# Kernel optimization log

Measured on AMD Instinct MI355X. Metric: run time of the kernel, lower is better.

The kernel has to match this reference:

```python
import jax, jax.numpy as jnp
import numpy as np

B, N, C, E, K, L = 8, 20000, 256, 320000, 3, 2
EPS = 1e-5

def setup_inputs() -> dict:
    key = jax.random.key(0)
    ks = jax.random.split(key, 8)
    features = jax.random.normal(ks[0], (B * N, C), dtype=jnp.float32)
    edge_index = jax.random.randint(ks[1], (2, E), 0, N, dtype=jnp.int64)
    # ChebConv params per layer: K linear weights [C,C] (no per-lin bias) + one bias [C]
    W = jax.random.normal(ks[2], (L, K, C, C), dtype=jnp.float32) * 0.05
    b = jax.random.normal(ks[3], (L, C), dtype=jnp.float32) * 0.05
    # node-mode LayerNorm affine params per layer
    ln_w = jnp.ones((L, C), dtype=jnp.float32)
    ln_b = jnp.zeros((L, C), dtype=jnp.float32)
    return {"features": features, "W": W, "b": b, "ln_w": ln_w, "ln_b": ln_b,
            "edge_index": edge_index, "batch_size": B}


def reference(features, W, b, ln_w, ln_b, edge_index, batch_size):
    n = features.shape[0] // batch_size
    c = features.shape[-1]
    src, dst = edge_index[0], edge_index[1]
    # sym-normalized Laplacian, lambda_max=2: L_hat = 2L/lmax - I = -D^-1/2 A D^-1/2
    deg = jax.ops.segment_sum(jnp.ones_like(src, dtype=features.dtype), src, num_segments=n)
    dis = jnp.where(deg > 0, jax.lax.rsqrt(jnp.where(deg > 0, deg, 1.0)), 0.0)
    norm = -dis[src] * dis[dst]  # [E]
    n_layers, k_order = W.shape[0], W.shape[1]

    def prop(x):  # L_hat @ x via gather-scale-scatter
        return jax.ops.segment_sum(norm[:, None] * x[src], dst, num_segments=n)

    def cheb(x, Wl, bl):
        Tx0 = x
        out = Tx0 @ Wl[0]
        Tx1 = prop(Tx0)
        out = out + Tx1 @ Wl[1]
        for k in range(2, k_order):
            Tx2 = 2.0 * prop(Tx1) - Tx0
            out = out + Tx2 @ Wl[k]
            Tx0, Tx1 = Tx1, Tx2
        return out + bl

    def single(feats):  # [n, c] -> [n, c]
        x = feats
        for i in range(n_layers):
            # NOTE: module passes original features to every layer's conv (faithful)
            x = cheb(feats, W[i], b[i])
            mu = jnp.mean(x, axis=-1, keepdims=True)
            var = jnp.var(x, axis=-1, keepdims=True)
            x = (x - mu) * jax.lax.rsqrt(var + EPS) * ln_w[i] + ln_b[i]
            # dropout p=0.0 -> identity
        return x

    fb = features.reshape(batch_size, n, c)
    return jax.vmap(single)(fb)
```

## Files before the change

### kernel.cpp

```cpp
#include <hip/hip_runtime.h>
#include <stdint.h>

#define BB 8
#define NN 20000
#define CC 256
#define EE 320000
#define KK 3
#define MROWS (BB * NN)
#define ROWU (BB * CC)

__device__ __forceinline__ float bf2f(ushort u) {
    union { uint32_t ui; float f; } v; v.ui = ((uint32_t)u) << 16; return v.f;
}
__device__ __forceinline__ ushort f2bf(float f) {
    union { uint32_t ui; float f; } v; v.f = f;
    uint32_t r = (v.ui + 0x7FFFu + ((v.ui >> 16) & 1u)) >> 16;
    return (ushort)r;
}

typedef __bf16 bf16x8 __attribute__((ext_vector_type(8)));
typedef float  f32x4  __attribute__((ext_vector_type(4)));

__device__ __forceinline__ void gload16(const void* gptr, void* lptr) {
    __builtin_amdgcn_global_load_lds(
        (const __attribute__((address_space(1))) void*)gptr,
        (__attribute__((address_space(3))) void*)lptr, 16, 0, 0);
}

__global__ void detect_k(const int* __restrict__ raw, int* __restrict__ flag) {
    int i = blockIdx.x * 256 + threadIdx.x;
    int v = 0;
    int idx = 2 * i + 1;
    if (i < EE) v = raw[idx];
    unsigned long long m = __ballot(v != 0);
    if ((threadIdx.x & 63) == 0 && m) atomicOr(flag, 1);
}

__global__ void convcount_k(const int* __restrict__ raw, const int* __restrict__ flag,
                            int mode,
                            int* __restrict__ src, int* __restrict__ dst,
                            int* __restrict__ deg_out, int* __restrict__ cnt_in) {
    int e = blockIdx.x * 256 + threadIdx.x;
    if (e >= EE) return;
    int m = mode ? mode : (*flag ? 1 : 2);
    int s, d;
    if (m == 2) { s = raw[2 * e]; d = raw[2 * EE + 2 * e]; }
    else        { s = raw[e];     d = raw[EE + e]; }
    src[e] = s; dst[e] = d;
    atomicAdd(&deg_out[s], 1);
    atomicAdd(&cnt_in[d], 1);
}

__global__ void __launch_bounds__(1024) scan_k(const int* __restrict__ cnt_in,
                                               const int* __restrict__ deg_out,
                                               int* __restrict__ row_ptr,
                                               float* __restrict__ dis) {
    __shared__ int wpart[16];
    const int t = threadIdx.x;
    const int lane = t & 63, wid = t >> 6;
    const int base = t * 20;
    int local[20];
    int sum = 0;
#pragma unroll
    for (int i = 0; i < 20; i++) {
        int idx = base + i;
        int v = (idx < NN) ? cnt_in[idx] : 0;
        local[i] = sum;
        sum += v;
    }
    int sc = sum;
#pragma unroll
    for (int off = 1; off < 64; off <<= 1) {
        int u = __shfl_up(sc, off, 64);
        if (lane >= off) sc += u;
    }
    if (lane == 63) wpart[wid] = sc;
    __syncthreads();
    if (wid == 0 && lane < 16) {
        int v = wpart[lane];
#pragma unroll
        for (int off = 1; off < 16; off <<= 1) {
            int u = __shfl_up(v, off, 64);
            if (lane >= off) v += u;
        }
        wpart[lane] = v;
    }
    __syncthreads();
    int wbase = (wid > 0) ? wpart[wid - 1] : 0;
    int tbase = wbase + sc - sum;
#pragma unroll
    for (int i = 0; i < 20; i++) {
        int idx = base + i;
        if (idx < NN) row_ptr[idx] = tbase + local[i];
    }
    if (t == 1023) row_ptr[NN] = tbase + sum;
    for (int i = t; i < NN; i += 1024) {
        int d = deg_out[i];
        dis[i] = (d > 0) ? rsqrtf((float)d) : 0.0f;
    }
}

__global__ void fill_k(const int* __restrict__ src, const int* __restrict__ dst,
                       const int* __restrict__ row_ptr, int* __restrict__ fillc,
                       const float* __restrict__ dis,
                       int2* __restrict__ cw) {
    int e = blockIdx.x * 256 + threadIdx.x;
    if (e >= EE) return;
    int s = src[e], d = dst[e];
    int pos = row_ptr[d] + atomicAdd(&fillc[d], 1);
    cw[pos] = make_int2(s, __float_as_int(-dis[s] * dis[d]));
}

__global__ void cvtwprep_k(const float* __restrict__ x, ushort* __restrict__ y,
                           const float* __restrict__ W, ushort* __restrict__ wt) {
    int bid = blockIdx.x;
    if (bid < MROWS * CC / 1024) {
        size_t idx = ((size_t)bid * 256 + threadIdx.x) * 4;
        int row = (int)(idx >> 8);
        int c = (int)(idx & 255);
        int b = row / NN, n = row - b * NN;
        float4 v = *(const float4*)(x + idx);
        ushort4 o = make_ushort4(f2bf(v.x), f2bf(v.y), f2bf(v.z), f2bf(v.w));
        *(ushort4*)(y + ((size_t)(n * BB + b) * CC + c)) = o;
    } else {
        int idx = (bid - MROWS * CC / 1024) * 256 + threadIdx.x;
        if (idx >= 256 * 768) return;
        int n = idx / 768, k = idx % 768;
        int sel = k >> 8, kk = k & 255;
        const float* W1 = W + KK * CC * CC;
        float v;
        if (sel == 0)      v = W1[kk * CC + n] - W1[2 * CC * CC + kk * CC + n];
        else if (sel == 1) v = W1[CC * CC + kk * CC + n];
        else               v = 2.0f * W1[2 * CC * CC + kk * CC + n];
        wt[idx] = f2bf(v);
    }
}

__global__ void __launch_bounds__(256) prop_k(const ushort* __restrict__ x,
                                              ushort* __restrict__ y,
                                              const int* __restrict__ row_ptr,
                                              const int2* __restrict__ cw) {
    const int n = blockIdx.x;
    const int t = threadIdx.x;
    const int beg = row_ptr[n], end = row_ptr[n + 1];
    const ushort* xb = x + t * 8;
    float a0 = 0, a1 = 0, a2 = 0, a3 = 0, a4 = 0, a5 = 0, a6 = 0, a7 = 0;
    int j = beg;
    for (; j + 4 <= end; j += 4) {
        int2 e0 = cw[j], e1 = cw[j + 1], e2 = cw[j + 2], e3 = cw[j + 3];
        int s0 = e0.x, s1 = e1.x, s2 = e2.x, s3 = e3.x;
        float w0 = __int_as_float(e0.y), w1 = __int_as_float(e1.y);
        float w2 = __int_as_float(e2.y), w3 = __int_as_float(e3.y);
        uint4 v0 = *(const uint4*)(xb + (size_t)s0 * ROWU);
        uint4 v1 = *(const uint4*)(xb + (size_t)s1 * ROWU);
        uint4 v2 = *(const uint4*)(xb + (size_t)s2 * ROWU);
        uint4 v3 = *(const uint4*)(xb + (size_t)s3 * ROWU);
        a0 += w0 * bf2f((ushort)v0.x) + w1 * bf2f((ushort)v1.x) + w2 * bf2f((ushort)v2.x) + w3 * bf2f((ushort)v3.x);
        a1 += w0 * bf2f((ushort)(v0.x >> 16)) + w1 * bf2f((ushort)(v1.x >> 16)) + w2 * bf2f((ushort)(v2.x >> 16)) + w3 * bf2f((ushort)(v3.x >> 16));
        a2 += w0 * bf2f((ushort)v0.y) + w1 * bf2f((ushort)v1.y) + w2 * bf2f((ushort)v2.y) + w3 * bf2f((ushort)v3.y);
        a3 += w0 * bf2f((ushort)(v0.y >> 16)) + w1 * bf2f((ushort)(v1.y >> 16)) + w2 * bf2f((ushort)(v2.y >> 16)) + w3 * bf2f((ushort)(v3.y >> 16));
        a4 += w0 * bf2f((ushort)v0.z) + w1 * bf2f((ushort)v1.z) + w2 * bf2f((ushort)v2.z) + w3 * bf2f((ushort)v3.z);
        a5 += w0 * bf2f((ushort)(v0.z >> 16)) + w1 * bf2f((ushort)(v1.z >> 16)) + w2 * bf2f((ushort)(v2.z >> 16)) + w3 * bf2f((ushort)(v3.z >> 16));
        a6 += w0 * bf2f((ushort)v0.w) + w1 * bf2f((ushort)v1.w) + w2 * bf2f((ushort)v2.w) + w3 * bf2f((ushort)v3.w);
        a7 += w0 * bf2f((ushort)(v0.w >> 16)) + w1 * bf2f((ushort)(v1.w >> 16)) + w2 * bf2f((ushort)(v2.w >> 16)) + w3 * bf2f((ushort)(v3.w >> 16));
    }
    for (; j < end; j++) {
        int2 e0 = cw[j];
        int s = e0.x;
        float wt = __int_as_float(e0.y);
        uint4 v = *(const uint4*)(xb + (size_t)s * ROWU);
        a0 += wt * bf2f((ushort)v.x);
        a1 += wt * bf2f((ushort)(v.x >> 16));
        a2 += wt * bf2f((ushort)v.y);
        a3 += wt * bf2f((ushort)(v.y >> 16));
        a4 += wt * bf2f((ushort)v.z);
        a5 += wt * bf2f((ushort)(v.z >> 16));
        a6 += wt * bf2f((ushort)v.w);
        a7 += wt * bf2f((ushort)(v.w >> 16));
    }
    uint4 o;
    o.x = (uint32_t)f2bf(a0) | ((uint32_t)f2bf(a1) << 16);
    o.y = (uint32_t)f2bf(a2) | ((uint32_t)f2bf(a3) << 16);
    o.z = (uint32_t)f2bf(a4) | ((uint32_t)f2bf(a5) << 16);
    o.w = (uint32_t)f2bf(a6) | ((uint32_t)f2bf(a7) << 16);
    *(uint4*)(y + (size_t)n * ROWU + t * 8) = o;
}

#define STAGE(buf, kt_) do {                                                   \
    const ushort* ab_ = ((kt_) < 8) ? a0 : (((kt_) < 16) ? a1 : a2);           \
    const int kl_ = ((kt_) & 7) * 32;                                          \
    const int kg_ = (kt_) * 32;                                                \
    gload16(ab_ + (size_t)(row0 + (tid >> 2)) * CC + kl_ + (tid & 3) * 8,      \
            &As[buf][wid * 512]);                                              \
    gload16(wt + (size_t)(tid >> 2) * 768 + kg_ + (tid & 3) * 8,               \
            &Bs[buf][wid * 512]);                                              \
    gload16(wt + (size_t)((512 + tid) >> 2) * 768 + kg_ + (tid & 3) * 8,       \
            &Bs[buf][4096 + wid * 512]);                                       \
} while (0)

__global__ void __launch_bounds__(512, 4) gemmln_k(const ushort* __restrict__ a0,
                                                   const ushort* __restrict__ a1,
                                                   const ushort* __restrict__ a2,
                                                   const ushort* __restrict__ wt,
                                                   const float* __restrict__ bias,
                                                   const float* __restrict__ lnw,
                                                   const float* __restrict__ lnb,
                                                   float* __restrict__ out) {
    __shared__ ushort As[2][128 * 32];
    __shared__ ushort Bs[2][256 * 32];
    __shared__ float reds[128][4];
    __shared__ float redq[128][4];
    const int tid = threadIdx.x;
    const int wid = tid >> 6, lane = tid & 63;
    const int wrow = wid >> 2, wcol = wid & 3;
    const int quad = lane >> 4, l16 = lane & 15;
    const int row0 = blockIdx.x * 128;

    f32x4 acc[4][4] = {};

    STAGE(0, 0);
    __syncthreads();
    int cur = 0;
    for (int kt = 0; kt < 24; kt++) {
        if (kt < 23) STAGE(cur ^ 1, kt + 1);

        bf16x8 af[4], bfr[4];
#pragma unroll
        for (int mt = 0; mt < 4; mt++)
            af[mt] = *(const bf16x8*)&As[cur][(wrow * 64 + mt * 16 + l16) * 32 + quad * 8];
#pragma unroll
        for (int nt = 0; nt < 4; nt++)
            bfr[nt] = *(const bf16x8*)&Bs[cur][(wcol * 64 + nt * 16 + l16) * 32 + quad * 8];
#pragma unroll
        for (int mt = 0; mt < 4; mt++)
#pragma unroll
            for (int nt = 0; nt < 4; nt++)
                acc[mt][nt] = __builtin_amdgcn_mfma_f32_16x16x32_bf16(
                    af[mt], bfr[nt], acc[mt][nt], 0, 0, 0);

        __syncthreads();
        cur ^= 1;
    }

    float bv[4], lwv[4], lbv[4];
#pragma unroll
    for (int nt = 0; nt < 4; nt++) {
        int c = wcol * 64 + nt * 16 + l16;
        bv[nt] = bias[c]; lwv[nt] = lnw[c]; lbv[nt] = lnb[c];
    }
#pragma unroll
    for (int mt = 0; mt < 4; mt++) {
#pragma unroll
        for (int r = 0; r < 4; r++) {
            float s = 0.0f, q = 0.0f;
#pragma unroll
            for (int nt = 0; nt < 4; nt++) {
                float v = acc[mt][nt][r] + bv[nt];
                s += v; q += v * v;
            }
#pragma unroll
            for (int off = 1; off < 16; off <<= 1) {
                s += __shfl_xor(s, off, 64);
                q += __shfl_xor(q, off, 64);
            }
            if (l16 == 0) {
                int ml = wrow * 64 + mt * 16 + quad * 4 + r;
                reds[ml][wcol] = s;
                redq[ml][wcol] = q;
            }
        }
    }
    __syncthreads();
#pragma unroll
    for (int mt = 0; mt < 4; mt++) {
#pragma unroll
        for (int r = 0; r < 4; r++) {
            int ml = wrow * 64 + mt * 16 + quad * 4 + r;
            float s = reds[ml][0] + reds[ml][1] + reds[ml][2] + reds[ml][3];
            float q = redq[ml][0] + redq[ml][1] + redq[ml][2] + redq[ml][3];
            float mean = s * (1.0f / CC);
            float var = q * (1.0f / CC) - mean * mean;
            float rs = rsqrtf(var + 1e-5f);
            int m = row0 + ml;
            int n = m >> 3, b = m & 7;
            size_t orow = (size_t)b * NN + n;
#pragma unroll
            for (int nt = 0; nt < 4; nt++) {
                int c = wcol * 64 + nt * 16 + l16;
                float v = (acc[mt][nt][r] + bv[nt] - mean) * rs * lwv[nt] + lbv[nt];
                out[orow * CC + c] = v;
            }
        }
    }
}

extern "C" void kernel_launch(void* const* d_in, const int* in_sizes, int n_in,
                              void* d_out, int out_size, void* d_ws, size_t ws_size,
                              hipStream_t stream) {
    const float* feats = (const float*)d_in[0];
    const float* W     = (const float*)d_in[1];
    const float* bvec  = (const float*)d_in[2];
    const float* lnw   = (const float*)d_in[3];
    const float* lnb   = (const float*)d_in[4];
    const int*   eidx  = (const int*)d_in[5];
    float* outp = (float*)d_out;

    int* flag    = (int*)d_ws;
    int* deg_out = flag + 64;
    int* cnt_in  = deg_out + NN;
    int* fillc   = cnt_in + NN;
    int* row_ptr = fillc + NN;
    int* srcw    = row_ptr + (NN + 64);
    int* dstw    = srcw + EE;
    int2* cw     = (int2*)(dstw + EE);
    float* disw  = (float*)(cw + EE);
    uintptr_t bf_base = ((uintptr_t)(disw + NN + 64) + 255) & ~(uintptr_t)255;
    ushort* featsb = (ushort*)bf_base;
    ushort* tx1b   = featsb + (size_t)MROWS * CC;
    ushort* p2b    = tx1b + (size_t)MROWS * CC;
    ushort* wcat   = p2b + (size_t)MROWS * CC;

    hipMemsetAsync(flag, 0, (size_t)(64 + 3 * NN) * sizeof(int), stream);

    int mode = 0;
    long long esz = in_sizes ? (long long)in_sizes[5] : 0;
    if (esz == (long long)2 * EE * 8) mode = 2;
    else if (esz == (long long)2 * EE * 4) mode = 1;

    int eb = (EE + 255) / 256;
    if (mode == 0) detect_k<<<eb, 256, 0, stream>>>(eidx, flag);
    convcount_k<<<eb, 256, 0, stream>>>(eidx, flag, mode, srcw, dstw, deg_out, cnt_in);
    scan_k<<<1, 1024, 0, stream>>>(cnt_in, deg_out, row_ptr, disw);
    fill_k<<<eb, 256, 0, stream>>>(srcw, dstw, row_ptr, fillc, disw, cw);

    cvtwprep_k<<<MROWS * CC / 1024 + 768, 256, 0, stream>>>(feats, featsb, W, wcat);

    prop_k<<<NN, 256, 0, stream>>>(featsb, tx1b, row_ptr, cw);
    prop_k<<<NN, 256, 0, stream>>>(tx1b, p2b, row_ptr, cw);

    gemmln_k<<<MROWS / 128, 512, 0, stream>>>(featsb, tx1b, p2b, wcat,
                                              bvec + CC, lnw + CC, lnb + CC, outp);
}
```

Before: 911.2 us.

## Switch bf16 activations to batch-major layout and fuse preprocessing kernels

Node activations now stay in the original batch-major [B][N][C] layout instead of being interleaved node-major [N][B][C]. The propagation kernel is restructured to one wavefront per (node, batch) pair on a 2D grid, with each lane gathering 8 bytes per neighbor instead of 16. The edge conversion/degree counting, feature bf16 conversion and weight prep are merged into a single launch, and the GEMM epilogue writes rows directly. The old node-major layout let each neighbor gather pull all batches as one contiguous 4 KB row. The new layout trades that for 512-byte gathers per neighbor and rereads the edge list once per batch, in exchange for a simpler transpose-free conversion and one fewer launch.

```diff
diff --git a/kernel.cpp b/kernel.cpp
--- a/kernel.cpp
+++ b/kernel.cpp
@@ -7,7 +7,6 @@
 #define EE 320000
 #define KK 3
 #define MROWS (BB * NN)
-#define ROWU (BB * CC)
 
 __device__ __forceinline__ float bf2f(ushort u) {
     union { uint32_t ui; float f; } v; v.ui = ((uint32_t)u) << 16; return v.f;
@@ -36,19 +35,39 @@
     if ((threadIdx.x & 63) == 0 && m) atomicOr(flag, 1);
 }
 
-__global__ void convcount_k(const int* __restrict__ raw, const int* __restrict__ flag,
-                            int mode,
-                            int* __restrict__ src, int* __restrict__ dst,
-                            int* __restrict__ deg_out, int* __restrict__ cnt_in) {
-    int e = blockIdx.x * 256 + threadIdx.x;
-    if (e >= EE) return;
-    int m = mode ? mode : (*flag ? 1 : 2);
-    int s, d;
-    if (m == 2) { s = raw[2 * e]; d = raw[2 * EE + 2 * e]; }
-    else        { s = raw[e];     d = raw[EE + e]; }
-    src[e] = s; dst[e] = d;
-    atomicAdd(&deg_out[s], 1);
-    atomicAdd(&cnt_in[d], 1);
+__global__ void fusedpre_k(const int* __restrict__ raw, const int* __restrict__ flag,
+                           int mode,
+                           int* __restrict__ src, int* __restrict__ dst,
+                           int* __restrict__ deg_out, int* __restrict__ cnt_in,
+                           const float* __restrict__ xf, ushort* __restrict__ xb,
+                           const float* __restrict__ W, ushort* __restrict__ wt) {
+    int bid = blockIdx.x;
+    if (bid < 1250) {
+        int e = bid * 256 + threadIdx.x;
+        if (e >= EE) return;
+        int m = mode ? mode : (*flag ? 1 : 2);
+        int s, d;
+        if (m == 2) { s = raw[2 * e]; d = raw[2 * EE + 2 * e]; }
+        else        { s = raw[e];     d = raw[EE + e]; }
+        src[e] = s; dst[e] = d;
+        atomicAdd(&deg_out[s], 1);
+        atomicAdd(&cnt_in[d], 1);
+    } else if (bid < 41250) {
+        size_t idx = ((size_t)(bid - 1250) * 256 + threadIdx.x) * 4;
+        float4 v = *(const float4*)(xf + idx);
+        *(ushort4*)(xb + idx) = make_ushort4(f2bf(v.x), f2bf(v.y), f2bf(v.z), f2bf(v.w));
+    } else {
+        int idx = (bid - 41250) * 256 + threadIdx.x;
+        if (idx >= 256 * 768) return;
+        int n = idx / 768, k = idx % 768;
+        int sel = k >> 8, kk = k & 255;
+        const float* W1 = W + KK * CC * CC;
+        float v;
+        if (sel == 0)      v = W1[kk * CC + n] - W1[2 * CC * CC + kk * CC + n];
+        else if (sel == 1) v = W1[CC * CC + kk * CC + n];
+        else               v = 2.0f * W1[2 * CC * CC + kk * CC + n];
+        wt[idx] = f2bf(v);
+    }
 }
 
 __global__ void __launch_bounds__(1024) scan_k(const int* __restrict__ cnt_in,
@@ -111,79 +130,47 @@
     cw[pos] = make_int2(s, __float_as_int(-dis[s] * dis[d]));
 }
 
-__global__ void cvtwprep_k(const float* __restrict__ x, ushort* __restrict__ y,
-                           const float* __restrict__ W, ushort* __restrict__ wt) {
-    int bid = blockIdx.x;
-    if (bid < MROWS * CC / 1024) {
-        size_t idx = ((size_t)bid * 256 + threadIdx.x) * 4;
-        int row = (int)(idx >> 8);
-        int c = (int)(idx & 255);
-        int b = row / NN, n = row - b * NN;
-        float4 v = *(const float4*)(x + idx);
-        ushort4 o = make_ushort4(f2bf(v.x), f2bf(v.y), f2bf(v.z), f2bf(v.w));
-        *(ushort4*)(y + ((size_t)(n * BB + b) * CC + c)) = o;
-    } else {
-        int idx = (bid - MROWS * CC / 1024) * 256 + threadIdx.x;
-        if (idx >= 256 * 768) return;
-        int n = idx / 768, k = idx % 768;
-        int sel = k >> 8, kk = k & 255;
-        const float* W1 = W + KK * CC * CC;
-        float v;
-        if (sel == 0)      v = W1[kk * CC + n] - W1[2 * CC * CC + kk * CC + n];
-        else if (sel == 1) v = W1[CC * CC + kk * CC + n];
-        else               v = 2.0f * W1[2 * CC * CC + kk * CC + n];
-        wt[idx] = f2bf(v);
-    }
-}
-
 __global__ void __launch_bounds__(256) prop_k(const ushort* __restrict__ x,
                                               ushort* __restrict__ y,
                                               const int* __restrict__ row_ptr,
                                               const int2* __restrict__ cw) {
-    const int n = blockIdx.x;
-    const int t = threadIdx.x;
+    const int wavei = threadIdx.x >> 6;
+    const int lane = threadIdx.x & 63;
+    const int n = blockIdx.x * 4 + wavei;
+    const int b = blockIdx.y;
+    const size_t bbase = (size_t)b * NN * CC;
+    const ushort* xb = x + bbase + lane * 4;
     const int beg = row_ptr[n], end = row_ptr[n + 1];
-    const ushort* xb = x + t * 8;
-    float a0 = 0, a1 = 0, a2 = 0, a3 = 0, a4 = 0, a5 = 0, a6 = 0, a7 = 0;
+    float a0 = 0, a1 = 0, a2 = 0, a3 = 0;
     int j = beg;
     for (; j + 4 <= end; j += 4) {
         int2 e0 = cw[j], e1 = cw[j + 1], e2 = cw[j + 2], e3 = cw[j + 3];
-        int s0 = e0.x, s1 = e1.x, s2 = e2.x, s3 = e3.x;
         float w0 = __int_as_float(e0.y), w1 = __int_as_float(e1.y);
         float w2 = __int_as_float(e2.y), w3 = __int_as_float(e3.y);
-        uint4 v0 = *(const uint4*)(xb + (size_t)s0 * ROWU);
-        uint4 v1 = *(const uint4*)(xb + (size_t)s1 * ROWU);
-        uint4 v2 = *(const uint4*)(xb + (size_t)s2 * ROWU);
-        uint4 v3 = *(const uint4*)(xb + (size_t)s3 * ROWU);
-        a0 += w0 * bf2f((ushort)v0.x) + w1 * bf2f((ushort)v1.x) + w2 * bf2f((ushort)v2.x) + w3 * bf2f((ushort)v3.x);
-        a1 += w0 * bf2f((ushort)(v0.x >> 16)) + w1 * bf2f((ushort)(v1.x >> 16)) + w2 * bf2f((ushort)(v2.x >> 16)) + w3 * bf2f((ushort)(v3.x >> 16));
-        a2 += w0 * bf2f((ushort)v0.y) + w1 * bf2f((ushort)v1.y) + w2 * bf2f((ushort)v2.y) + w3 * bf2f((ushort)v3.y);
-        a3 += w0 * bf2f((ushort)(v0.y >> 16)) + w1 * bf2f((ushort)(v1.y >> 16)) + w2 * bf2f((ushort)(v2.y >> 16)) + w3 * bf2f((ushort)(v3.y >> 16));
-        a4 += w0 * bf2f((ushort)v0.z) + w1 * bf2f((ushort)v1.z) + w2 * bf2f((ushort)v2.z) + w3 * bf2f((ushort)v3.z);
-        a5 += w0 * bf2f((ushort)(v0.z >> 16)) + w1 * bf2f((ushort)(v1.z >> 16)) + w2 * bf2f((ushort)(v2.z >> 16)) + w3 * bf2f((ushort)(v3.z >> 16));
-        a6 += w0 * bf2f((ushort)v0.w) + w1 * bf2f((ushort)v1.w) + w2 * bf2f((ushort)v2.w) + w3 * bf2f((ushort)v3.w);
-        a7 += w0 * bf2f((ushort)(v0.w >> 16)) + w1 * bf2f((ushort)(v1.w >> 16)) + w2 * bf2f((ushort)(v2.w >> 16)) + w3 * bf2f((ushort)(v3.w >> 16));
+        uint2 v0 = *(const uint2*)(xb + (size_t)e0.x * CC);
+        uint2 v1 = *(const uint2*)(xb + (size_t)e1.x * CC);
+        uint2 v2 = *(const uint2*)(xb + (size_t)e2.x * CC);
+        uint2 v3 = *(const uint2*)(xb + (size_t)e3.x * CC);
+        a0 += w0 * bf2f((ushort)v0.x) + w1 * bf2f((ushort)v1.x)
+            + w2 * bf2f((ushort)v2.x) + w3 * bf2f((ushort)v3.x);
+        a1 += w0 * bf2f((ushort)(v0.x >> 16)) + w1 * bf2f((ushort)(v1.x >> 16))
+            + w2 * bf2f((ushort)(v2.x >> 16)) + w3 * bf2f((ushort)(v3.x >> 16));
+        a2 += w0 * bf2f((ushort)v0.y) + w1 * bf2f((ushort)v1.y)
+            + w2 * bf2f((ushort)v2.y) + w3 * bf2f((ushort)v3.y);
+        a3 += w0 * bf2f((ushort)(v0.y >> 16)) + w1 * bf2f((ushort)(v1.y >> 16))
+            + w2 * bf2f((ushort)(v2.y >> 16)) + w3 * bf2f((ushort)(v3.y >> 16));
     }
     for (; j < end; j++) {
         int2 e0 = cw[j];
-        int s = e0.x;
         float wt = __int_as_float(e0.y);
-        uint4 v = *(const uint4*)(xb + (size_t)s * ROWU);
+        uint2 v = *(const uint2*)(xb + (size_t)e0.x * CC);
         a0 += wt * bf2f((ushort)v.x);
         a1 += wt * bf2f((ushort)(v.x >> 16));
         a2 += wt * bf2f((ushort)v.y);
         a3 += wt * bf2f((ushort)(v.y >> 16));
-        a4 += wt * bf2f((ushort)v.z);
-        a5 += wt * bf2f((ushort)(v.z >> 16));
-        a6 += wt * bf2f((ushort)v.w);
-        a7 += wt * bf2f((ushort)(v.w >> 16));
-    }
-    uint4 o;
-    o.x = (uint32_t)f2bf(a0) | ((uint32_t)f2bf(a1) << 16);
-    o.y = (uint32_t)f2bf(a2) | ((uint32_t)f2bf(a3) << 16);
-    o.z = (uint32_t)f2bf(a4) | ((uint32_t)f2bf(a5) << 16);
-    o.w = (uint32_t)f2bf(a6) | ((uint32_t)f2bf(a7) << 16);
-    *(uint4*)(y + (size_t)n * ROWU + t * 8) = o;
+    }
+    ushort4 o = make_ushort4(f2bf(a0), f2bf(a1), f2bf(a2), f2bf(a3));
+    *(ushort4*)(y + bbase + (size_t)n * CC + lane * 4) = o;
 }
 
 #define STAGE(buf, kt_) do {                                                   \
@@ -281,9 +268,7 @@
             float mean = s * (1.0f / CC);
             float var = q * (1.0f / CC) - mean * mean;
             float rs = rsqrtf(var + 1e-5f);
-            int m = row0 + ml;
-            int n = m >> 3, b = m & 7;
-            size_t orow = (size_t)b * NN + n;
+            size_t orow = (size_t)(row0 + ml);
 #pragma unroll
             for (int nt = 0; nt < 4; nt++) {
                 int c = wcol * 64 + nt * 16 + l16;
@@ -329,14 +314,15 @@
 
     int eb = (EE + 255) / 256;
     if (mode == 0) detect_k<<<eb, 256, 0, stream>>>(eidx, flag);
-    convcount_k<<<eb, 256, 0, stream>>>(eidx, flag, mode, srcw, dstw, deg_out, cnt_in);
+
+    fusedpre_k<<<1250 + 40000 + 768, 256, 0, stream>>>(eidx, flag, mode,
+                                                       srcw, dstw, deg_out, cnt_in,
+                                                       feats, featsb, W, wcat);
     scan_k<<<1, 1024, 0, stream>>>(cnt_in, deg_out, row_ptr, disw);
     fill_k<<<eb, 256, 0, stream>>>(srcw, dstw, row_ptr, fillc, disw, cw);
 
-    cvtwprep_k<<<MROWS * CC / 1024 + 768, 256, 0, stream>>>(feats, featsb, W, wcat);
-
-    prop_k<<<NN, 256, 0, stream>>>(featsb, tx1b, row_ptr, cw);
-    prop_k<<<NN, 256, 0, stream>>>(tx1b, p2b, row_ptr, cw);
+    prop_k<<<dim3(NN / 4, BB), 256, 0, stream>>>(featsb, tx1b, row_ptr, cw);
+    prop_k<<<dim3(NN / 4, BB), 256, 0, stream>>>(tx1b, p2b, row_ptr, cw);
 
     gemmln_k<<<MROWS / 128, 512, 0, stream>>>(featsb, tx1b, p2b, wcat,
                                               bvec + CC, lnw + CC, lnb + CC, outp);
```

New measurement: 797.8 us. -12.4%, faster.
